# Performance work log

Hardware: AMD Instinct MI355X
Metric: run time of the kernel (lower is better)

Reference implementation:

```python
import jax, jax.numpy as jnp
import numpy as np

O, P, G, N, H, D = 3, 128, 64, 20000, 512, 128
TEMPERATURE = 0.1
EPS = 1e-12


def setup_inputs() -> dict:
    key = jax.random.key(0)
    k0, k1, k2, k3 = jax.random.split(key, 4)
    emb = jax.random.normal(k0, (O, N, H), dtype=jnp.float32)
    idx = jax.random.randint(k1, (O, P, G), 0, N)
    W1 = jax.random.normal(k2, (O, H, H), dtype=jnp.float32) * 0.02
    b1 = jnp.zeros((O, H), dtype=jnp.float32)
    W2 = jax.random.normal(k3, (O, H, D), dtype=jnp.float32) * 0.02
    b2 = jnp.zeros((O, D), dtype=jnp.float32)
    return {"emb": emb, "W1": W1, "b1": b1, "W2": W2, "b2": b2, "idx": idx}


def reference(emb, W1, b1, W2, b2, idx):
    # Per-omics pathway prototypes: gather gene rows then mean-pool.  [O,P,H]
    protos = jax.vmap(lambda e, i: jnp.mean(e[i], axis=1))(emb, idx)
    # Per-omics projection head: Linear -> ReLU -> (Dropout=identity in eval) -> Linear
    h = jax.nn.relu(jnp.einsum('oph,ohk->opk', protos, W1) + b1[:, None, :])
    z = jnp.einsum('opk,okd->opd', h, W2) + b2[:, None, :]          # [O,P,D]
    # Original loops p outer, ntype inner -> order (pathway, omics)
    z = jnp.transpose(z, (1, 0, 2)).reshape(P * O, D)                # [M,D], M=P*O
    z = z / (jnp.linalg.norm(z, axis=-1, keepdims=True) + EPS)       # l2 normalize
    y = jnp.repeat(jnp.arange(P), O)                                 # pathway labels [M]

    sim = (z @ z.T) / TEMPERATURE                                    # [M,M]
    M = sim.shape[0]
    eye = jnp.eye(M, dtype=bool)
    sim = jnp.where(eye, -jnp.inf, sim)
    pos_mask = (y[None, :] == y[:, None]) & ~eye
    exp_sim = jnp.exp(sim)                                           # exp(-inf)=0 on diagonal
    denom = exp_sim.sum(axis=1) + EPS
    pos_sum = jnp.sum(exp_sim * pos_mask.astype(exp_sim.dtype), axis=1) + EPS
    # every anchor has O-1 positives here, so all anchors are valid
    loss = -jnp.log(pos_sum / denom)
    return loss.mean()
```

## Files before the change

kernel.cpp:

```cpp
#include <hip/hip_runtime.h>
#include <math.h>

#define O_ 3
#define P_ 128
#define G_ 64
#define N_ 20000
#define H_ 512
#define D_ 128
#define M_ (O_*P_)

static constexpr float TEMP_INV = 10.0f;
static constexpr float EPS_ = 1e-12f;

__global__ __launch_bounds__(512) void k_protos(const float* __restrict__ emb,
                                                const int* __restrict__ idx,
                                                float* __restrict__ protos) {
    const int b = blockIdx.x;
    const int o = b >> 7;
    const int t = threadIdx.x;
    const int q = t >> 7, c4 = t & 127;

    __shared__ int sIdx[G_];
    __shared__ float4 sRed[4][128];

    if (t < G_) sIdx[t] = idx[b * G_ + t];
    __syncthreads();

    const float* base = emb + (size_t)o * N_ * H_ + (size_t)c4 * 4;
    float4 acc = make_float4(0.f, 0.f, 0.f, 0.f);
    #pragma unroll
    for (int g = 0; g < 16; ++g) {
        const float4 v = *(const float4*)(base + (size_t)((unsigned)sIdx[q * 16 + g]) * H_);
        acc.x += v.x; acc.y += v.y; acc.z += v.z; acc.w += v.w;
    }
    sRed[q][c4] = acc;
    __syncthreads();

    if (q == 0) {
        const float4 a0 = sRed[0][c4], a1 = sRed[1][c4];
        const float4 a2 = sRed[2][c4], a3 = sRed[3][c4];
        const float s = 1.0f / (float)G_;
        float4 r;
        r.x = (a0.x + a1.x + a2.x + a3.x) * s;
        r.y = (a0.y + a1.y + a2.y + a3.y) * s;
        r.z = (a0.z + a1.z + a2.z + a3.z) * s;
        r.w = (a0.w + a1.w + a2.w + a3.w) * s;
        ((float4*)(protos + (size_t)b * H_))[c4] = r;
    }
}

#define PRSTR 516
__global__ __launch_bounds__(512) void k_gemm1(const float* __restrict__ protos,
                                               const float* __restrict__ W1,
                                               const float* __restrict__ b1,
                                               float* __restrict__ hbuf) {
    const int blk = blockIdx.x;
    const int o = blk >> 7;
    const int rem = blk & 127;
    const int pg = rem >> 3, ks = rem & 7;
    const int p0 = pg * 8, k0 = ks * 64;
    const int t = threadIdx.x;
    const int hs = t >> 7, r = (t >> 4) & 7, q4 = t & 15;

    __shared__ float sPr[8 * PRSTR];
    __shared__ float4 sPart[4][8][16];

    {
        const float4* src = (const float4*)(protos + (size_t)(o * P_ + p0) * H_);
        #pragma unroll
        for (int i = 0; i < 2; ++i) {
            const int fidx = i * 512 + t;
            const int rr = fidx >> 7, c4 = fidx & 127;
            ((float4*)sPr)[rr * (PRSTR / 4) + c4] = src[rr * 128 + c4];
        }
    }
    __syncthreads();

    const float4* w1 = (const float4*)(W1 + (size_t)o * H_ * H_) + (k0 >> 2) + q4;
    const float* pr = sPr + r * PRSTR + hs * 128;
    float4 acc = make_float4(0.f, 0.f, 0.f, 0.f);
    #pragma unroll 8
    for (int h = 0; h < 128; ++h) {
        const float a = pr[h];
        const float4 w = w1[(size_t)(hs * 128 + h) * 128];
        acc.x = fmaf(a, w.x, acc.x);
        acc.y = fmaf(a, w.y, acc.y);
        acc.z = fmaf(a, w.z, acc.z);
        acc.w = fmaf(a, w.w, acc.w);
    }
    sPart[hs][r][q4] = acc;
    __syncthreads();

    if (hs == 0) {
        const float4 r0 = sPart[0][r][q4], r1 = sPart[1][r][q4];
        const float4 r2 = sPart[2][r][q4], r3 = sPart[3][r][q4];
        const float4 bb = ((const float4*)(b1 + (size_t)o * H_ + k0))[q4];
        float4 out;
        out.x = fmaxf(r0.x + r1.x + r2.x + r3.x + bb.x, 0.f);
        out.y = fmaxf(r0.y + r1.y + r2.y + r3.y + bb.y, 0.f);
        out.z = fmaxf(r0.z + r1.z + r2.z + r3.z + bb.z, 0.f);
        out.w = fmaxf(r0.w + r1.w + r2.w + r3.w + bb.w, 0.f);
        ((float4*)(hbuf + (size_t)(o * P_ + p0 + r) * H_ + k0))[q4] = out;
    }
}

__global__ __launch_bounds__(512) void k_gemm2_norm(const float* __restrict__ hbuf,
                                                    const float* __restrict__ W2,
                                                    const float* __restrict__ b2,
                                                    float* __restrict__ z) {
    const int b = blockIdx.x;
    const int o = b >> 7, p = b & 127;
    const int t = threadIdx.x;
    const int ks = t >> 5, dq = t & 31;

    __shared__ float sH[H_];
    __shared__ float4 sPart[16][32];
    __shared__ float sZ[D_];
    __shared__ float sNr[2];

    sH[t] = hbuf[(size_t)b * H_ + t];
    __syncthreads();

    const float4* w2 = (const float4*)(W2 + (size_t)o * H_ * D_) + dq;
    float4 acc = make_float4(0.f, 0.f, 0.f, 0.f);
    const int h0 = ks * 32;
    #pragma unroll 8
    for (int h = 0; h < 32; ++h) {
        const float a = sH[h0 + h];
        const float4 w = w2[(size_t)(h0 + h) * 32];
        acc.x = fmaf(a, w.x, acc.x);
        acc.y = fmaf(a, w.y, acc.y);
        acc.z = fmaf(a, w.z, acc.z);
        acc.w = fmaf(a, w.w, acc.w);
    }
    sPart[ks][dq] = acc;
    __syncthreads();

    if (t < 32) {
        float4 s = make_float4(0.f, 0.f, 0.f, 0.f);
        #pragma unroll
        for (int j = 0; j < 16; ++j) {
            const float4 v = sPart[j][t];
            s.x += v.x; s.y += v.y; s.z += v.z; s.w += v.w;
        }
        const float4 bb = ((const float4*)(b2 + (size_t)o * D_))[t];
        s.x += bb.x; s.y += bb.y; s.z += bb.z; s.w += bb.w;
        ((float4*)sZ)[t] = s;
    }
    __syncthreads();

    if (t < D_) {
        const float v = sZ[t];
        float s = v * v;
        #pragma unroll
        for (int off = 32; off > 0; off >>= 1) s += __shfl_down(s, off, 64);
        if ((t & 63) == 0) sNr[t >> 6] = s;
    }
    __syncthreads();
    if (t < D_) {
        const float inv = 1.0f / (sqrtf(sNr[0] + sNr[1]) + EPS_);
        z[(size_t)(p * O_ + o) * D_ + t] = sZ[t] * inv;
    }
}

__global__ __launch_bounds__(256) void k_loss(const float* __restrict__ z,
                                              float* __restrict__ out) {
    const int i = blockIdx.x;
    const int t = threadIdx.x;
    __shared__ float zi[D_];
    if (t < D_) zi[t] = z[(size_t)i * D_ + t];
    __syncthreads();
    const int pi = i / 3;
    float denom = 0.f, pos = 0.f;
    const float4* zi4 = (const float4*)zi;
    #pragma unroll
    for (int jj = 0; jj < 2; ++jj) {
        const int j = t + jj * 256;
        if (j < M_) {
            const float4* zj = (const float4*)(z + (size_t)j * D_);
            float dot = 0.f;
            #pragma unroll 8
            for (int q = 0; q < D_ / 4; ++q) {
                const float4 a = zi4[q];
                const float4 bb = zj[q];
                dot = fmaf(a.x, bb.x, fmaf(a.y, bb.y, fmaf(a.z, bb.z, fmaf(a.w, bb.w, dot))));
            }
            if (j != i) {
                const float e = __expf(dot * TEMP_INV);
                denom += e;
                if (j / 3 == pi) pos += e;
            }
        }
    }
    #pragma unroll
    for (int off = 32; off > 0; off >>= 1) {
        denom += __shfl_down(denom, off, 64);
        pos   += __shfl_down(pos,   off, 64);
    }
    __shared__ float rd[4], rp[4];
    const int lane = t & 63, wid = t >> 6;
    if (lane == 0) { rd[wid] = denom; rp[wid] = pos; }
    __syncthreads();
    if (t == 0) {
        const float dn = rd[0] + rd[1] + rd[2] + rd[3] + EPS_;
        const float ps = rp[0] + rp[1] + rp[2] + rp[3] + EPS_;
        const float loss_i = logf(dn) - logf(ps);
        atomicAdd(out, loss_i * (1.0f / (float)M_));
    }
}

extern "C" void kernel_launch(void* const* d_in, const int* in_sizes, int n_in,
                              void* d_out, int out_size, void* d_ws, size_t ws_size,
                              hipStream_t stream) {
    const float* emb = (const float*)d_in[0];
    const float* W1  = (const float*)d_in[1];
    const float* b1  = (const float*)d_in[2];
    const float* W2  = (const float*)d_in[3];
    const float* b2  = (const float*)d_in[4];
    const int*   idx = (const int*)d_in[5];

    float* ws     = (float*)d_ws;
    float* protos = ws;
    float* hbuf   = ws + 196608;
    float* zbuf   = ws + 393216;

    hipMemsetAsync(d_out, 0, sizeof(float), stream);

    k_protos    <<<dim3(M_), dim3(512), 0, stream>>>(emb, idx, protos);
    k_gemm1     <<<dim3(M_), dim3(512), 0, stream>>>(protos, W1, b1, hbuf);
    k_gemm2_norm<<<dim3(M_), dim3(512), 0, stream>>>(hbuf, W2, b2, zbuf);
    k_loss      <<<dim3(M_), dim3(256), 0, stream>>>(zbuf, (float*)d_out);
}
```

Before: 219.7 us.

## Fuse four stage kernels into one persistent kernel with grid barriers

Merges the prototype gather, first GEMM, second GEMM with normalization, and contrastive loss into a single kernel of 384 blocks. Stages are separated by atomic-counter grid barriers in workspace memory, which are zeroed by an extra memset. This removes three kernel launch gaps. In exchange it relies on all 384 blocks being co-resident and adds spin-wait barrier cost. The barrier gives up after a bounded spin count, so if blocks are not co-resident it can proceed before earlier stages finish and give wrong results. The loss stage is rewritten for 512 threads with one j per thread.

```diff
diff --git a/kernel.cpp b/kernel.cpp
--- a/kernel.cpp
+++ b/kernel.cpp
@@ -8,176 +8,191 @@
 #define H_ 512
 #define D_ 128
 #define M_ (O_*P_)
+#define PRSTR 516
 
 static constexpr float TEMP_INV = 10.0f;
 static constexpr float EPS_ = 1e-12f;
 
-__global__ __launch_bounds__(512) void k_protos(const float* __restrict__ emb,
-                                                const int* __restrict__ idx,
-                                                float* __restrict__ protos) {
-    const int b = blockIdx.x;
-    const int o = b >> 7;
+__device__ __forceinline__ void gbar(unsigned* cnt) {
+    __syncthreads();
+    if (threadIdx.x == 0) {
+        __threadfence();
+        __hip_atomic_fetch_add(cnt, 1u, __ATOMIC_ACQ_REL, __HIP_MEMORY_SCOPE_AGENT);
+        unsigned spins = 0;
+        while (__hip_atomic_load(cnt, __ATOMIC_ACQUIRE, __HIP_MEMORY_SCOPE_AGENT) < (unsigned)M_) {
+            __builtin_amdgcn_s_sleep(8);
+            if (++spins > (1u << 20)) break;
+        }
+    }
+    __syncthreads();
+    __threadfence();
+}
+
+__global__ __launch_bounds__(512) void k_all(const float* __restrict__ emb,
+                                             const int* __restrict__ idx,
+                                             const float* __restrict__ W1,
+                                             const float* __restrict__ b1,
+                                             const float* __restrict__ W2,
+                                             const float* __restrict__ b2,
+                                             float* __restrict__ protos,
+                                             float* __restrict__ hbuf,
+                                             float* __restrict__ zbuf,
+                                             float* __restrict__ out,
+                                             unsigned* __restrict__ bars) {
+    const int blk = blockIdx.x;
     const int t = threadIdx.x;
-    const int q = t >> 7, c4 = t & 127;
-
-    __shared__ int sIdx[G_];
-    __shared__ float4 sRed[4][128];
-
-    if (t < G_) sIdx[t] = idx[b * G_ + t];
-    __syncthreads();
-
-    const float* base = emb + (size_t)o * N_ * H_ + (size_t)c4 * 4;
-    float4 acc = make_float4(0.f, 0.f, 0.f, 0.f);
-    #pragma unroll
-    for (int g = 0; g < 16; ++g) {
-        const float4 v = *(const float4*)(base + (size_t)((unsigned)sIdx[q * 16 + g]) * H_);
-        acc.x += v.x; acc.y += v.y; acc.z += v.z; acc.w += v.w;
-    }
-    sRed[q][c4] = acc;
-    __syncthreads();
-
-    if (q == 0) {
-        const float4 a0 = sRed[0][c4], a1 = sRed[1][c4];
-        const float4 a2 = sRed[2][c4], a3 = sRed[3][c4];
-        const float s = 1.0f / (float)G_;
-        float4 r;
-        r.x = (a0.x + a1.x + a2.x + a3.x) * s;
-        r.y = (a0.y + a1.y + a2.y + a3.y) * s;
-        r.z = (a0.z + a1.z + a2.z + a3.z) * s;
-        r.w = (a0.w + a1.w + a2.w + a3.w) * s;
-        ((float4*)(protos + (size_t)b * H_))[c4] = r;
-    }
-}
-
-#define PRSTR 516
-__global__ __launch_bounds__(512) void k_gemm1(const float* __restrict__ protos,
-                                               const float* __restrict__ W1,
-                                               const float* __restrict__ b1,
-                                               float* __restrict__ hbuf) {
-    const int blk = blockIdx.x;
-    const int o = blk >> 7;
-    const int rem = blk & 127;
-    const int pg = rem >> 3, ks = rem & 7;
-    const int p0 = pg * 8, k0 = ks * 64;
-    const int t = threadIdx.x;
-    const int hs = t >> 7, r = (t >> 4) & 7, q4 = t & 15;
-
-    __shared__ float sPr[8 * PRSTR];
-    __shared__ float4 sPart[4][8][16];
-
-    {
-        const float4* src = (const float4*)(protos + (size_t)(o * P_ + p0) * H_);
+
+    __shared__ __align__(16) char smem[24832];
+
+    {
+        int*    sIdx = (int*)smem;
+        float4* sRed = (float4*)(smem + 256);
+        const int o = blk >> 7;
+        const int q = t >> 7, c4 = t & 127;
+
+        if (t < G_) sIdx[t] = idx[blk * G_ + t];
+        __syncthreads();
+
+        const float* base = emb + (size_t)o * N_ * H_ + (size_t)c4 * 4;
+        float4 acc = make_float4(0.f, 0.f, 0.f, 0.f);
         #pragma unroll
-        for (int i = 0; i < 2; ++i) {
-            const int fidx = i * 512 + t;
-            const int rr = fidx >> 7, c4 = fidx & 127;
-            ((float4*)sPr)[rr * (PRSTR / 4) + c4] = src[rr * 128 + c4];
-        }
-    }
-    __syncthreads();
-
-    const float4* w1 = (const float4*)(W1 + (size_t)o * H_ * H_) + (k0 >> 2) + q4;
-    const float* pr = sPr + r * PRSTR + hs * 128;
-    float4 acc = make_float4(0.f, 0.f, 0.f, 0.f);
-    #pragma unroll 8
-    for (int h = 0; h < 128; ++h) {
-        const float a = pr[h];
-        const float4 w = w1[(size_t)(hs * 128 + h) * 128];
-        acc.x = fmaf(a, w.x, acc.x);
-        acc.y = fmaf(a, w.y, acc.y);
-        acc.z = fmaf(a, w.z, acc.z);
-        acc.w = fmaf(a, w.w, acc.w);
-    }
-    sPart[hs][r][q4] = acc;
-    __syncthreads();
-
-    if (hs == 0) {
-        const float4 r0 = sPart[0][r][q4], r1 = sPart[1][r][q4];
-        const float4 r2 = sPart[2][r][q4], r3 = sPart[3][r][q4];
-        const float4 bb = ((const float4*)(b1 + (size_t)o * H_ + k0))[q4];
-        float4 out;
-        out.x = fmaxf(r0.x + r1.x + r2.x + r3.x + bb.x, 0.f);
-        out.y = fmaxf(r0.y + r1.y + r2.y + r3.y + bb.y, 0.f);
-        out.z = fmaxf(r0.z + r1.z + r2.z + r3.z + bb.z, 0.f);
-        out.w = fmaxf(r0.w + r1.w + r2.w + r3.w + bb.w, 0.f);
-        ((float4*)(hbuf + (size_t)(o * P_ + p0 + r) * H_ + k0))[q4] = out;
-    }
-}
-
-__global__ __launch_bounds__(512) void k_gemm2_norm(const float* __restrict__ hbuf,
-                                                    const float* __restrict__ W2,
-                                                    const float* __restrict__ b2,
-                                                    float* __restrict__ z) {
-    const int b = blockIdx.x;
-    const int o = b >> 7, p = b & 127;
-    const int t = threadIdx.x;
-    const int ks = t >> 5, dq = t & 31;
-
-    __shared__ float sH[H_];
-    __shared__ float4 sPart[16][32];
-    __shared__ float sZ[D_];
-    __shared__ float sNr[2];
-
-    sH[t] = hbuf[(size_t)b * H_ + t];
-    __syncthreads();
-
-    const float4* w2 = (const float4*)(W2 + (size_t)o * H_ * D_) + dq;
-    float4 acc = make_float4(0.f, 0.f, 0.f, 0.f);
-    const int h0 = ks * 32;
-    #pragma unroll 8
-    for (int h = 0; h < 32; ++h) {
-        const float a = sH[h0 + h];
-        const float4 w = w2[(size_t)(h0 + h) * 32];
-        acc.x = fmaf(a, w.x, acc.x);
-        acc.y = fmaf(a, w.y, acc.y);
-        acc.z = fmaf(a, w.z, acc.z);
-        acc.w = fmaf(a, w.w, acc.w);
-    }
-    sPart[ks][dq] = acc;
-    __syncthreads();
-
-    if (t < 32) {
-        float4 s = make_float4(0.f, 0.f, 0.f, 0.f);
-        #pragma unroll
-        for (int j = 0; j < 16; ++j) {
-            const float4 v = sPart[j][t];
-            s.x += v.x; s.y += v.y; s.z += v.z; s.w += v.w;
-        }
-        const float4 bb = ((const float4*)(b2 + (size_t)o * D_))[t];
-        s.x += bb.x; s.y += bb.y; s.z += bb.z; s.w += bb.w;
-        ((float4*)sZ)[t] = s;
-    }
-    __syncthreads();
-
-    if (t < D_) {
-        const float v = sZ[t];
-        float s = v * v;
-        #pragma unroll
-        for (int off = 32; off > 0; off >>= 1) s += __shfl_down(s, off, 64);
-        if ((t & 63) == 0) sNr[t >> 6] = s;
-    }
-    __syncthreads();
-    if (t < D_) {
-        const float inv = 1.0f / (sqrtf(sNr[0] + sNr[1]) + EPS_);
-        z[(size_t)(p * O_ + o) * D_ + t] = sZ[t] * inv;
-    }
-}
-
-__global__ __launch_bounds__(256) void k_loss(const float* __restrict__ z,
-                                              float* __restrict__ out) {
-    const int i = blockIdx.x;
-    const int t = threadIdx.x;
-    __shared__ float zi[D_];
-    if (t < D_) zi[t] = z[(size_t)i * D_ + t];
-    __syncthreads();
-    const int pi = i / 3;
-    float denom = 0.f, pos = 0.f;
-    const float4* zi4 = (const float4*)zi;
-    #pragma unroll
-    for (int jj = 0; jj < 2; ++jj) {
-        const int j = t + jj * 256;
-        if (j < M_) {
-            const float4* zj = (const float4*)(z + (size_t)j * D_);
+        for (int g = 0; g < 16; ++g) {
+            const float4 v = *(const float4*)(base + (size_t)((unsigned)sIdx[q * 16 + g]) * H_);
+            acc.x += v.x; acc.y += v.y; acc.z += v.z; acc.w += v.w;
+        }
+        sRed[q * 128 + c4] = acc;
+        __syncthreads();
+
+        if (q == 0) {
+            const float4 a0 = sRed[0 * 128 + c4], a1 = sRed[1 * 128 + c4];
+            const float4 a2 = sRed[2 * 128 + c4], a3 = sRed[3 * 128 + c4];
+            const float s = 1.0f / (float)G_;
+            float4 r;
+            r.x = (a0.x + a1.x + a2.x + a3.x) * s;
+            r.y = (a0.y + a1.y + a2.y + a3.y) * s;
+            r.z = (a0.z + a1.z + a2.z + a3.z) * s;
+            r.w = (a0.w + a1.w + a2.w + a3.w) * s;
+            ((float4*)(protos + (size_t)blk * H_))[c4] = r;
+        }
+    }
+    gbar(bars + 0);
+
+    {
+        float*  sPr   = (float*)smem;
+        float4* sPart = (float4*)(smem + 16512);
+        const int o = blk >> 7;
+        const int rem = blk & 127;
+        const int pg = rem >> 3, ks = rem & 7;
+        const int p0 = pg * 8, k0 = ks * 64;
+        const int hs = t >> 7, r = (t >> 4) & 7, q4 = t & 15;
+
+        {
+            const float4* src = (const float4*)(protos + (size_t)(o * P_ + p0) * H_);
+            #pragma unroll
+            for (int i = 0; i < 2; ++i) {
+                const int fidx = i * 512 + t;
+                const int rr = fidx >> 7, c4 = fidx & 127;
+                ((float4*)sPr)[rr * (PRSTR / 4) + c4] = src[rr * 128 + c4];
+            }
+        }
+        __syncthreads();
+
+        const float4* w1 = (const float4*)(W1 + (size_t)o * H_ * H_) + (k0 >> 2) + q4;
+        const float* pr = sPr + r * PRSTR + hs * 128;
+        float4 acc = make_float4(0.f, 0.f, 0.f, 0.f);
+        #pragma unroll 8
+        for (int h = 0; h < 128; ++h) {
+            const float a = pr[h];
+            const float4 w = w1[(size_t)(hs * 128 + h) * 128];
+            acc.x = fmaf(a, w.x, acc.x);
+            acc.y = fmaf(a, w.y, acc.y);
+            acc.z = fmaf(a, w.z, acc.z);
+            acc.w = fmaf(a, w.w, acc.w);
+        }
+        sPart[(hs * 8 + r) * 16 + q4] = acc;
+        __syncthreads();
+
+        if (hs == 0) {
+            const float4 r0 = sPart[(0 * 8 + r) * 16 + q4], r1 = sPart[(1 * 8 + r) * 16 + q4];
+            const float4 r2 = sPart[(2 * 8 + r) * 16 + q4], r3 = sPart[(3 * 8 + r) * 16 + q4];
+            const float4 bb = ((const float4*)(b1 + (size_t)o * H_ + k0))[q4];
+            float4 o4;
+            o4.x = fmaxf(r0.x + r1.x + r2.x + r3.x + bb.x, 0.f);
+            o4.y = fmaxf(r0.y + r1.y + r2.y + r3.y + bb.y, 0.f);
+            o4.z = fmaxf(r0.z + r1.z + r2.z + r3.z + bb.z, 0.f);
+            o4.w = fmaxf(r0.w + r1.w + r2.w + r3.w + bb.w, 0.f);
+            ((float4*)(hbuf + (size_t)(o * P_ + p0 + r) * H_ + k0))[q4] = o4;
+        }
+    }
+    gbar(bars + 1);
+
+    {
+        float*  sH    = (float*)smem;
+        float4* sPart = (float4*)(smem + 2048);
+        float*  sZ    = (float*)(smem + 10240);
+        float*  sNr   = (float*)(smem + 10752);
+        const int o = blk >> 7, p = blk & 127;
+        const int ks = t >> 5, dq = t & 31;
+
+        sH[t] = hbuf[(size_t)blk * H_ + t];
+        __syncthreads();
+
+        const float4* w2 = (const float4*)(W2 + (size_t)o * H_ * D_) + dq;
+        float4 acc = make_float4(0.f, 0.f, 0.f, 0.f);
+        const int h0 = ks * 32;
+        #pragma unroll 8
+        for (int h = 0; h < 32; ++h) {
+            const float a = sH[h0 + h];
+            const float4 w = w2[(size_t)(h0 + h) * 32];
+            acc.x = fmaf(a, w.x, acc.x);
+            acc.y = fmaf(a, w.y, acc.y);
+            acc.z = fmaf(a, w.z, acc.z);
+            acc.w = fmaf(a, w.w, acc.w);
+        }
+        sPart[ks * 32 + dq] = acc;
+        __syncthreads();
+
+        if (t < 32) {
+            float4 s = make_float4(0.f, 0.f, 0.f, 0.f);
+            #pragma unroll
+            for (int j = 0; j < 16; ++j) {
+                const float4 v = sPart[j * 32 + t];
+                s.x += v.x; s.y += v.y; s.z += v.z; s.w += v.w;
+            }
+            const float4 bb = ((const float4*)(b2 + (size_t)o * D_))[t];
+            s.x += bb.x; s.y += bb.y; s.z += bb.z; s.w += bb.w;
+            ((float4*)sZ)[t] = s;
+        }
+        __syncthreads();
+
+        if (t < D_) {
+            const float v = sZ[t];
+            float s = v * v;
+            #pragma unroll
+            for (int off = 32; off > 0; off >>= 1) s += __shfl_down(s, off, 64);
+            if ((t & 63) == 0) sNr[t >> 6] = s;
+        }
+        __syncthreads();
+        if (t < D_) {
+            const float inv = 1.0f / (sqrtf(sNr[0] + sNr[1]) + EPS_);
+            zbuf[(size_t)(p * O_ + o) * D_ + t] = sZ[t] * inv;
+        }
+    }
+    gbar(bars + 2);
+
+    {
+        float* zi = (float*)smem;
+        float* rd = (float*)(smem + 512);
+        float* rp = (float*)(smem + 544);
+        const int i = blk;
+        if (t < D_) zi[t] = zbuf[(size_t)i * D_ + t];
+        __syncthreads();
+
+        const int pi = i / 3;
+        float denom = 0.f, pos = 0.f;
+        if (t < M_) {
+            const float4* zi4 = (const float4*)zi;
+            const float4* zj  = (const float4*)(zbuf + (size_t)t * D_);
             float dot = 0.f;
             #pragma unroll 8
             for (int q = 0; q < D_ / 4; ++q) {
@@ -185,27 +200,27 @@
                 const float4 bb = zj[q];
                 dot = fmaf(a.x, bb.x, fmaf(a.y, bb.y, fmaf(a.z, bb.z, fmaf(a.w, bb.w, dot))));
             }
-            if (j != i) {
+            if (t != i) {
                 const float e = __expf(dot * TEMP_INV);
-                denom += e;
-                if (j / 3 == pi) pos += e;
-            }
-        }
-    }
-    #pragma unroll
-    for (int off = 32; off > 0; off >>= 1) {
-        denom += __shfl_down(denom, off, 64);
-        pos   += __shfl_down(pos,   off, 64);
-    }
-    __shared__ float rd[4], rp[4];
-    const int lane = t & 63, wid = t >> 6;
-    if (lane == 0) { rd[wid] = denom; rp[wid] = pos; }
-    __syncthreads();
-    if (t == 0) {
-        const float dn = rd[0] + rd[1] + rd[2] + rd[3] + EPS_;
-        const float ps = rp[0] + rp[1] + rp[2] + rp[3] + EPS_;
-        const float loss_i = logf(dn) - logf(ps);
-        atomicAdd(out, loss_i * (1.0f / (float)M_));
+                denom = e;
+                if (t / 3 == pi) pos = e;
+            }
+        }
+        #pragma unroll
+        for (int off = 32; off > 0; off >>= 1) {
+            denom += __shfl_down(denom, off, 64);
+            pos   += __shfl_down(pos,   off, 64);
+        }
+        const int lane = t & 63, wid = t >> 6;
+        if (lane == 0) { rd[wid] = denom; rp[wid] = pos; }
+        __syncthreads();
+        if (t == 0) {
+            float dn = EPS_, ps = EPS_;
+            #pragma unroll
+            for (int w = 0; w < 8; ++w) { dn += rd[w]; ps += rp[w]; }
+            const float loss_i = logf(dn) - logf(ps);
+            atomicAdd(out, loss_i * (1.0f / (float)M_));
+        }
     }
 }
 
@@ -223,11 +238,12 @@
     float* protos = ws;
     float* hbuf   = ws + 196608;
     float* zbuf   = ws + 393216;
+    unsigned* bars = (unsigned*)(ws + 442368);
 
     hipMemsetAsync(d_out, 0, sizeof(float), stream);
-
-    k_protos    <<<dim3(M_), dim3(512), 0, stream>>>(emb, idx, protos);
-    k_gemm1     <<<dim3(M_), dim3(512), 0, stream>>>(protos, W1, b1, hbuf);
-    k_gemm2_norm<<<dim3(M_), dim3(512), 0, stream>>>(hbuf, W2, b2, zbuf);
-    k_loss      <<<dim3(M_), dim3(256), 0, stream>>>(zbuf, (float*)d_out);
+    hipMemsetAsync(bars, 0, 3 * sizeof(unsigned), stream);
+
+    k_all<<<dim3(M_), dim3(512), 0, stream>>>(emb, idx, W1, b1, W2, b2,
+                                              protos, hbuf, zbuf,
+                                              (float*)d_out, bars);
 }
```

New measurement: 545.6 us. +148.3%, slower.
